# Kernel optimization log

Hardware: AMD Instinct MI355X
Metric: run time of the kernel (lower is better)

## Reference

```python
import jax, jax.numpy as jnp
import numpy as np

BATCH = 32768
IN_DIM = 64
NUM_CLASSES = 4096


def setup_inputs() -> dict:
    key = jax.random.key(0)
    kx, kw = jax.random.split(key)
    x = jax.random.normal(kx, (BATCH, IN_DIM), dtype=jnp.float32)
    # prototypes are random +/-1 as in the torch module (randint(0,2)*2-1)
    w = (jax.random.randint(kw, (NUM_CLASSES, IN_DIM), 0, 2).astype(jnp.float32) * 2.0 - 1.0)
    return {"x": x, "w": w}


def reference(x, w):
    # logits[b, c] = -||x[b] - w[c]||^2
    x_sq = jnp.sum(x * x, axis=-1)          # [B]
    w_sq = jnp.sum(w * w, axis=-1)          # [C]
    cross = jnp.einsum('bd,cd->bc', x, w)   # [B, C]
    logits = 2.0 * cross - x_sq[:, None] - w_sq[None, :]
    return logits
```

## Files before the change

kernel.cpp:

```cpp
#include <hip/hip_runtime.h>
#include <hip/hip_bf16.h>

#define BATCH 32768
#define IN_DIM 64
#define NUM_CLASSES 4096

typedef short bf16x8 __attribute__((ext_vector_type(8)));
typedef float f32x4 __attribute__((ext_vector_type(4)));

__global__ void convert_rows(const float* __restrict__ src,
                             unsigned short* __restrict__ dst,
                             float* __restrict__ sq) {
    int t = blockIdx.x * blockDim.x + threadIdx.x;
    float4 v = ((const float4*)src)[t];

    __hip_bfloat16 h0 = __float2bfloat16(v.x);
    __hip_bfloat16 h1 = __float2bfloat16(v.y);
    __hip_bfloat16 h2 = __float2bfloat16(v.z);
    __hip_bfloat16 h3 = __float2bfloat16(v.w);
    ushort4 o;
    o.x = __builtin_bit_cast(unsigned short, h0);
    o.y = __builtin_bit_cast(unsigned short, h1);
    o.z = __builtin_bit_cast(unsigned short, h2);
    o.w = __builtin_bit_cast(unsigned short, h3);
    ((ushort4*)dst)[t] = o;

    float s = v.x * v.x + v.y * v.y + v.z * v.z + v.w * v.w;
    s += __shfl_xor(s, 1, 16);
    s += __shfl_xor(s, 2, 16);
    s += __shfl_xor(s, 4, 16);
    s += __shfl_xor(s, 8, 16);
    if ((threadIdx.x & 15) == 0) sq[t >> 4] = s;
}

__global__ __launch_bounds__(256) void rbf_gemm(
    const unsigned short* __restrict__ xb,
    const unsigned short* __restrict__ wb,
    const float* __restrict__ xsq,
    const float* __restrict__ wsq,
    float* __restrict__ out)
{
    const int bid    = blockIdx.x;
    const int tile_n = bid & 31;
    const int tile_m = bid >> 5;
    const int lane   = threadIdx.x & 63;
    const int wave   = threadIdx.x >> 6;
    const int wm     = wave >> 1;
    const int wn     = wave & 1;
    const int m0     = tile_m * 128 + wm * 64;
    const int n0     = tile_n * 128 + wn * 64;
    const int r      = lane & 15;
    const int quad   = lane >> 4;

    const unsigned short* arow = xb + (size_t)(m0 + r) * IN_DIM + quad * 8;
    const unsigned short* brow = wb + (size_t)(n0 + r) * IN_DIM + quad * 8;

    bf16x8 a[4][2], b[4][2];
#pragma unroll
    for (int i = 0; i < 4; ++i) {
#pragma unroll
        for (int s = 0; s < 2; ++s) {
            a[i][s] = *(const bf16x8*)(arow + i * 16 * IN_DIM + s * 32);
            b[i][s] = *(const bf16x8*)(brow + i * 16 * IN_DIM + s * 32);
        }
    }

    f32x4 acc[4][4];
#pragma unroll
    for (int i = 0; i < 4; ++i)
#pragma unroll
        for (int j = 0; j < 4; ++j)
            acc[i][j] = (f32x4)0.0f;

#pragma unroll
    for (int s = 0; s < 2; ++s)
#pragma unroll
        for (int i = 0; i < 4; ++i)
#pragma unroll
            for (int j = 0; j < 4; ++j)
                acc[i][j] = __builtin_amdgcn_mfma_f32_16x16x32_bf16(
                    a[i][s], b[j][s], acc[i][j], 0, 0, 0);

    float wsq_r[4];
#pragma unroll
    for (int j = 0; j < 4; ++j) wsq_r[j] = wsq[n0 + j * 16 + r];

#pragma unroll
    for (int i = 0; i < 4; ++i) {
#pragma unroll
        for (int reg = 0; reg < 4; ++reg) {
            const int m = m0 + i * 16 + quad * 4 + reg;
            const float xs = xsq[m];
            float* obase = out + (size_t)m * NUM_CLASSES + n0 + r;
#pragma unroll
            for (int j = 0; j < 4; ++j)
                obase[j * 16] = 2.0f * acc[i][j][reg] - xs - wsq_r[j];
        }
    }
}

extern "C" void kernel_launch(void* const* d_in, const int* in_sizes, int n_in,
                              void* d_out, int out_size, void* d_ws, size_t ws_size,
                              hipStream_t stream) {
    const float* x = (const float*)d_in[0];
    const float* w = (const float*)d_in[1];
    float* out = (float*)d_out;

    char* ws = (char*)d_ws;
    unsigned short* xb = (unsigned short*)ws;
    unsigned short* wb = (unsigned short*)(ws + (size_t)BATCH * IN_DIM * 2);
    float* xsq = (float*)(ws + (size_t)BATCH * IN_DIM * 2
                             + (size_t)NUM_CLASSES * IN_DIM * 2);
    float* wsq = xsq + BATCH;

    convert_rows<<<(BATCH * IN_DIM / 4) / 256, 256, 0, stream>>>(x, xb, xsq);
    convert_rows<<<(NUM_CLASSES * IN_DIM / 4) / 256, 256, 0, stream>>>(w, wb, wsq);

    const int grid = (BATCH / 128) * (NUM_CLASSES / 128);
    rbf_gemm<<<grid, 256, 0, stream>>>(xb, wb, xsq, wsq, out);
}
```

Baseline: 564.7 us.

## Stage GEMM epilogue through swizzled LDS for coalesced 16-byte output stores

```diff
diff --git a/kernel.cpp b/kernel.cpp
--- a/kernel.cpp
+++ b/kernel.cpp
@@ -40,6 +40,8 @@
     const float* __restrict__ wsq,
     float* __restrict__ out)
 {
+    __shared__ float lds[4 * 2048];
+
     const int bid    = blockIdx.x;
     const int tile_n = bid & 31;
     const int tile_m = bid >> 5;
@@ -79,23 +81,48 @@
 #pragma unroll
             for (int j = 0; j < 4; ++j)
                 acc[i][j] = __builtin_amdgcn_mfma_f32_16x16x32_bf16(
-                    a[i][s], b[j][s], acc[i][j], 0, 0, 0);
+                    b[j][s], a[i][s], acc[i][j], 0, 0, 0);
 
-    float wsq_r[4];
+    float xs[4];
 #pragma unroll
-    for (int j = 0; j < 4; ++j) wsq_r[j] = wsq[n0 + j * 16 + r];
+    for (int i = 0; i < 4; ++i) xs[i] = xsq[m0 + i * 16 + r];
+
+    f32x4 wv[4];
+#pragma unroll
+    for (int j = 0; j < 4; ++j)
+        wv[j] = *(const f32x4*)(wsq + n0 + j * 16 + quad * 4);
+
+    char* my = (char*)(lds + wave * 2048);
 
 #pragma unroll
-    for (int i = 0; i < 4; ++i) {
+    for (int h = 0; h < 2; ++h) {
 #pragma unroll
-        for (int reg = 0; reg < 4; ++reg) {
-            const int m = m0 + i * 16 + quad * 4 + reg;
-            const float xs = xsq[m];
-            float* obase = out + (size_t)m * NUM_CLASSES + n0 + r;
+        for (int ii = 0; ii < 2; ++ii) {
+            const int i  = 2 * h + ii;
+            const int rl = ii * 16 + r;
+            const int swz = (rl & 7) << 4;
 #pragma unroll
-            for (int j = 0; j < 4; ++j)
-                obase[j * 16] = 2.0f * acc[i][j][reg] - xs - wsq_r[j];
+            for (int j = 0; j < 4; ++j) {
+                f32x4 v;
+                v[0] = 2.0f * acc[i][j][0] - xs[i] - wv[j][0];
+                v[1] = 2.0f * acc[i][j][1] - xs[i] - wv[j][1];
+                v[2] = 2.0f * acc[i][j][2] - xs[i] - wv[j][2];
+                v[3] = 2.0f * acc[i][j][3] - xs[i] - wv[j][3];
+                const int byte = rl * 256 + (((j * 4 + quad) * 16) ^ swz);
+                *(f32x4*)(my + byte) = v;
+            }
         }
+        __syncthreads();
+
+#pragma unroll
+        for (int p = 0; p < 8; ++p) {
+            const int rl  = p * 4 + quad;
+            const int swz = (rl & 7) << 4;
+            f32x4 v = *(const f32x4*)(my + rl * 256 + ((r * 16) ^ swz));
+            *(f32x4*)(out + (size_t)(m0 + h * 32 + rl) * NUM_CLASSES
+                          + n0 + r * 4) = v;
+        }
+        if (h == 0) __syncthreads();
     }
 }
 
```

Result: faster. 545.1 us (-3.5%).
